# Kernel optimization log

Hardware: AMD Instinct MI355X
Metric: run time of the kernel (lower is better)

The kernel has to match this reference:

```python
import jax, jax.numpy as jnp
import numpy as np

BATCH_SIZE = 2048
TEMPERATURE = 0.5
EPS = 1e-8  # torch CosineSimilarity eps


def setup_inputs() -> dict:
    key = jax.random.key(0)
    k1, k2 = jax.random.split(key)
    d = 512
    z_i = jax.random.normal(k1, (BATCH_SIZE, d), dtype=jnp.float32)
    z_j = jax.random.normal(k2, (BATCH_SIZE, d), dtype=jnp.float32)
    return {"z_i": z_i, "z_j": z_j}


def reference(z_i, z_j):
    B = BATCH_SIZE
    n = 2 * B
    z = jnp.concatenate([z_i, z_j], axis=0)              # [n, d]
    # cosine similarity via normalize + GEMM (same math as broadcasted CosineSimilarity)
    norms = jnp.maximum(jnp.linalg.norm(z, axis=1, keepdims=True), EPS)
    zn = z / norms                                       # [n, d]
    S = zn @ zn.T                                        # [n, n]
    # drop diagonal: row i keeps columns j != i, in order (matches sim[~eye].view(n, n-1))
    cols = jnp.arange(n - 1)[None, :]                    # [1, n-1]
    rows = jnp.arange(n)[:, None]                        # [n, 1]
    idx = cols + (cols >= rows)                          # skip diagonal
    off_diag = jnp.take_along_axis(S, idx, axis=1)       # [n, n-1]
    # positive pair: pos_pairs = cat(z_j, z_i) -> partner index (i + B) mod n
    pos = jnp.take_along_axis(S, ((rows[:, 0] + B) % n)[:, None], axis=1)  # [n, 1]
    logits = jnp.concatenate([pos, off_diag], axis=1) / TEMPERATURE        # [n, n]
    # cross-entropy with label 0, reduction='sum', then / n  == mean over rows
    loss = jnp.mean(jax.nn.logsumexp(logits, axis=1) - logits[:, 0])
    return loss
```

## Files before the change

kernel.cpp:

```cpp
#include <hip/hip_runtime.h>
#include <hip/hip_bf16.h>

#define N_TOT 4096
#define D     512
#define BHALF 2048

#define EXP2_SCALE 2.8853900817779268f
#define E2 7.3890560989306495f

typedef __attribute__((ext_vector_type(8))) short short8;
typedef __attribute__((ext_vector_type(4))) float floatx4;

#define AS_GLOBAL(p) ((const __attribute__((address_space(1))) void*)(p))
#define AS_LDS(p)    ((__attribute__((address_space(3))) void*)(p))

__global__ void normalize_kernel(const float* __restrict__ z_i,
                                 const float* __restrict__ z_j,
                                 short* __restrict__ zn,
                                 float* __restrict__ rowsum) {
    const int wave = threadIdx.x >> 6, lane = threadIdx.x & 63;
    const int row = blockIdx.x * 4 + wave;
    const float* src = (row < BHALF) ? (z_i + (size_t)row * D)
                                     : (z_j + (size_t)(row - BHALF) * D);
    if (lane == 0) rowsum[row] = 0.0f;
    float4 v0 = ((const float4*)src)[lane];
    float4 v1 = ((const float4*)src)[lane + 64];
    float ss = v0.x*v0.x + v0.y*v0.y + v0.z*v0.z + v0.w*v0.w
             + v1.x*v1.x + v1.y*v1.y + v1.z*v1.z + v1.w*v1.w;
    #pragma unroll
    for (int off = 32; off > 0; off >>= 1) ss += __shfl_xor(ss, off);
    float inv = 1.0f / fmaxf(sqrtf(ss), 1e-8f);
    short4 o0, o1;
    o0.x = (short)__bfloat16_as_ushort(__float2bfloat16(v0.x * inv));
    o0.y = (short)__bfloat16_as_ushort(__float2bfloat16(v0.y * inv));
    o0.z = (short)__bfloat16_as_ushort(__float2bfloat16(v0.z * inv));
    o0.w = (short)__bfloat16_as_ushort(__float2bfloat16(v0.w * inv));
    o1.x = (short)__bfloat16_as_ushort(__float2bfloat16(v1.x * inv));
    o1.y = (short)__bfloat16_as_ushort(__float2bfloat16(v1.y * inv));
    o1.z = (short)__bfloat16_as_ushort(__float2bfloat16(v1.z * inv));
    o1.w = (short)__bfloat16_as_ushort(__float2bfloat16(v1.w * inv));
    ((short4*)(zn + (size_t)row * D))[lane]      = o0;
    ((short4*)(zn + (size_t)row * D))[lane + 64] = o1;
}

__launch_bounds__(256)
__global__ void gemm_fused(const short* __restrict__ zn,
                           float* __restrict__ rowsum,
                           float* __restrict__ spos) {
    __shared__ short At[2][128 * 32];
    __shared__ short Bt[2][128 * 32];

    int b = blockIdx.x, bi = 0, rowlen = 32;
    while (b >= rowlen) { b -= rowlen; rowlen--; bi++; }
    const int bj = bi + b;
    const int i0 = bi * 128;
    const int j0 = bj * 128;

    const int t = threadIdx.x;
    const int lane = t & 63, wave = t >> 6;
    const int wm = wave & 1, wn = wave >> 1;
    const int quad = lane >> 4, l16 = lane & 15;

    const int sr = lane >> 2;
    const int sc = (lane & 3) * 8;
    const short* gA0 = zn + (size_t)(i0 + wave * 32 + sr)      * D + sc;
    const short* gA1 = zn + (size_t)(i0 + wave * 32 + 16 + sr) * D + sc;
    const short* gB0 = zn + (size_t)(j0 + wave * 32 + sr)      * D + sc;
    const short* gB1 = zn + (size_t)(j0 + wave * 32 + 16 + sr) * D + sc;
    const int lo0 = (wave * 32)      * 32;
    const int lo1 = (wave * 32 + 16) * 32;

    floatx4 acc[4][4] = {};

    __builtin_amdgcn_global_load_lds(AS_GLOBAL(gA0), AS_LDS(&At[0][lo0]), 16, 0, 0);
    __builtin_amdgcn_global_load_lds(AS_GLOBAL(gA1), AS_LDS(&At[0][lo1]), 16, 0, 0);
    __builtin_amdgcn_global_load_lds(AS_GLOBAL(gB0), AS_LDS(&Bt[0][lo0]), 16, 0, 0);
    __builtin_amdgcn_global_load_lds(AS_GLOBAL(gB1), AS_LDS(&Bt[0][lo1]), 16, 0, 0);

    for (int kt = 0; kt < 16; ++kt) {
        const int cur = kt & 1;
        __syncthreads();
        if (kt < 15) {
            const int nxt = 1 - cur;
            const int ko = (kt + 1) * 32;
            __builtin_amdgcn_global_load_lds(AS_GLOBAL(gA0 + ko), AS_LDS(&At[nxt][lo0]), 16, 0, 0);
            __builtin_amdgcn_global_load_lds(AS_GLOBAL(gA1 + ko), AS_LDS(&At[nxt][lo1]), 16, 0, 0);
            __builtin_amdgcn_global_load_lds(AS_GLOBAL(gB0 + ko), AS_LDS(&Bt[nxt][lo0]), 16, 0, 0);
            __builtin_amdgcn_global_load_lds(AS_GLOBAL(gB1 + ko), AS_LDS(&Bt[nxt][lo1]), 16, 0, 0);
        }
        short8 af[4], bf[4];
        #pragma unroll
        for (int tm = 0; tm < 4; ++tm)
            af[tm] = *(const short8*)(&At[cur][(wm*64 + tm*16 + l16) * 32 + quad*8]);
        #pragma unroll
        for (int tn = 0; tn < 4; ++tn)
            bf[tn] = *(const short8*)(&Bt[cur][(wn*64 + tn*16 + l16) * 32 + quad*8]);
        #pragma unroll
        for (int tm = 0; tm < 4; ++tm)
            #pragma unroll
            for (int tn = 0; tn < 4; ++tn)
                acc[tm][tn] = __builtin_amdgcn_mfma_f32_16x16x32_bf16(
                    af[tm], bf[tn], acc[tm][tn], 0, 0, 0);
    }

    float cs[4] = {0.f, 0.f, 0.f, 0.f};
    #pragma unroll
    for (int tm = 0; tm < 4; ++tm) {
        float rs[4] = {0.f, 0.f, 0.f, 0.f};
        #pragma unroll
        for (int tn = 0; tn < 4; ++tn)
            #pragma unroll
            for (int r = 0; r < 4; ++r) {
                float e = exp2f(acc[tm][tn][r] * EXP2_SCALE);
                rs[r] += e;
                cs[tn] += e;
            }
        #pragma unroll
        for (int r = 0; r < 4; ++r) {
            float v = rs[r];
            v += __shfl_xor(v, 1);
            v += __shfl_xor(v, 2);
            v += __shfl_xor(v, 4);
            v += __shfl_xor(v, 8);
            if (l16 == 0) {
                int gi = i0 + wm*64 + tm*16 + quad*4 + r;
                atomicAdd(&rowsum[gi], v);
            }
        }
    }
    if (bi != bj) {
        #pragma unroll
        for (int tn = 0; tn < 4; ++tn) {
            float v = cs[tn];
            v += __shfl_xor(v, 16);
            v += __shfl_xor(v, 32);
            if (quad == 0) {
                int gj = j0 + wn*64 + tn*16 + l16;
                atomicAdd(&rowsum[gj], v);
            }
        }
    }
    if (bj == bi + 16) {
        #pragma unroll
        for (int tm = 0; tm < 4; ++tm)
            #pragma unroll
            for (int tn = 0; tn < 4; ++tn)
                #pragma unroll
                for (int r = 0; r < 4; ++r) {
                    int li = wm*64 + tm*16 + quad*4 + r;
                    int lj = wn*64 + tn*16 + l16;
                    if (li == lj) {
                        float s = acc[tm][tn][r];
                        spos[i0 + li]         = s;
                        spos[i0 + li + BHALF] = s;
                    }
                }
    }
}

__global__ void finalize_kernel(const float* __restrict__ rowsum,
                                const float* __restrict__ spos,
                                float* __restrict__ out) {
    int t = threadIdx.x;
    float acc = 0.f;
    for (int i = t; i < N_TOT; i += 1024) {
        float sp = spos[i];
        float denom = rowsum[i] - E2 + exp2f(sp * EXP2_SCALE);
        acc += __logf(denom) - 2.0f * sp;
    }
    #pragma unroll
    for (int off = 32; off > 0; off >>= 1) acc += __shfl_xor(acc, off);
    __shared__ float red[16];
    if ((t & 63) == 0) red[t >> 6] = acc;
    __syncthreads();
    if (t == 0) {
        float s = 0.f;
        #pragma unroll
        for (int w = 0; w < 16; ++w) s += red[w];
        out[0] = s / (float)N_TOT;
    }
}

extern "C" void kernel_launch(void* const* d_in, const int* in_sizes, int n_in,
                              void* d_out, int out_size, void* d_ws, size_t ws_size,
                              hipStream_t stream) {
    const float* z_i = (const float*)d_in[0];
    const float* z_j = (const float*)d_in[1];
    float* out = (float*)d_out;

    char* ws = (char*)d_ws;
    short* zn     = (short*)ws;
    float* rowsum = (float*)(ws + (size_t)N_TOT * D * 2);
    float* spos   = rowsum + N_TOT;

    normalize_kernel<<<N_TOT / 4, 256, 0, stream>>>(z_i, z_j, zn, rowsum);
    gemm_fused<<<(32 * 33) / 2, 256, 0, stream>>>(zn, rowsum, spos);
    finalize_kernel<<<1, 1024, 0, stream>>>(rowsum, spos, out);
}
```

Before: 89.94 us.

## Quantize normalized embeddings to FP8 and use triple-buffered FP8 MFMA GEMM

```diff
diff --git a/kernel.cpp b/kernel.cpp
--- a/kernel.cpp
+++ b/kernel.cpp
@@ -8,15 +8,16 @@
 #define EXP2_SCALE 2.8853900817779268f
 #define E2 7.3890560989306495f
 
-typedef __attribute__((ext_vector_type(8))) short short8;
 typedef __attribute__((ext_vector_type(4))) float floatx4;
 
 #define AS_GLOBAL(p) ((const __attribute__((address_space(1))) void*)(p))
 #define AS_LDS(p)    ((__attribute__((address_space(3))) void*)(p))
 
+#define WAITCNT_VM(n) (0xF70 | (n))
+
 __global__ void normalize_kernel(const float* __restrict__ z_i,
                                  const float* __restrict__ z_j,
-                                 short* __restrict__ zn,
+                                 unsigned char* __restrict__ zn,
                                  float* __restrict__ rowsum) {
     const int wave = threadIdx.x >> 6, lane = threadIdx.x & 63;
     const int row = blockIdx.x * 4 + wave;
@@ -30,25 +31,21 @@
     #pragma unroll
     for (int off = 32; off > 0; off >>= 1) ss += __shfl_xor(ss, off);
     float inv = 1.0f / fmaxf(sqrtf(ss), 1e-8f);
-    short4 o0, o1;
-    o0.x = (short)__bfloat16_as_ushort(__float2bfloat16(v0.x * inv));
-    o0.y = (short)__bfloat16_as_ushort(__float2bfloat16(v0.y * inv));
-    o0.z = (short)__bfloat16_as_ushort(__float2bfloat16(v0.z * inv));
-    o0.w = (short)__bfloat16_as_ushort(__float2bfloat16(v0.w * inv));
-    o1.x = (short)__bfloat16_as_ushort(__float2bfloat16(v1.x * inv));
-    o1.y = (short)__bfloat16_as_ushort(__float2bfloat16(v1.y * inv));
-    o1.z = (short)__bfloat16_as_ushort(__float2bfloat16(v1.z * inv));
-    o1.w = (short)__bfloat16_as_ushort(__float2bfloat16(v1.w * inv));
-    ((short4*)(zn + (size_t)row * D))[lane]      = o0;
-    ((short4*)(zn + (size_t)row * D))[lane + 64] = o1;
+    int w0 = __builtin_amdgcn_cvt_pk_fp8_f32(v0.x * inv, v0.y * inv, 0, false);
+    w0     = __builtin_amdgcn_cvt_pk_fp8_f32(v0.z * inv, v0.w * inv, w0, true);
+    int w1 = __builtin_amdgcn_cvt_pk_fp8_f32(v1.x * inv, v1.y * inv, 0, false);
+    w1     = __builtin_amdgcn_cvt_pk_fp8_f32(v1.z * inv, v1.w * inv, w1, true);
+    int* dst = (int*)(zn + (size_t)row * D);
+    dst[lane]      = w0;
+    dst[lane + 64] = w1;
 }
 
 __launch_bounds__(256)
-__global__ void gemm_fused(const short* __restrict__ zn,
+__global__ void gemm_fused(const unsigned char* __restrict__ zn,
                            float* __restrict__ rowsum,
                            float* __restrict__ spos) {
-    __shared__ short At[2][128 * 32];
-    __shared__ short Bt[2][128 * 32];
+    __shared__ unsigned char At[3][128 * 32];
+    __shared__ unsigned char Bt[3][128 * 32];
 
     int b = blockIdx.x, bi = 0, rowlen = 32;
     while (b >= rowlen) { b -= rowlen; rowlen--; bi++; }
@@ -61,45 +58,44 @@
     const int wm = wave & 1, wn = wave >> 1;
     const int quad = lane >> 4, l16 = lane & 15;
 
-    const int sr = lane >> 2;
-    const int sc = (lane & 3) * 8;
-    const short* gA0 = zn + (size_t)(i0 + wave * 32 + sr)      * D + sc;
-    const short* gA1 = zn + (size_t)(i0 + wave * 32 + 16 + sr) * D + sc;
-    const short* gB0 = zn + (size_t)(j0 + wave * 32 + sr)      * D + sc;
-    const short* gB1 = zn + (size_t)(j0 + wave * 32 + 16 + sr) * D + sc;
-    const int lo0 = (wave * 32)      * 32;
-    const int lo1 = (wave * 32 + 16) * 32;
+    const int srow = wave * 32 + (lane >> 1);
+    const int scol = (lane & 1) * 16;
+    const unsigned char* gA = zn + (size_t)(i0 + srow) * D + scol;
+    const unsigned char* gB = zn + (size_t)(j0 + srow) * D + scol;
+    const int lo = srow * 32 + scol;
 
     floatx4 acc[4][4] = {};
 
-    __builtin_amdgcn_global_load_lds(AS_GLOBAL(gA0), AS_LDS(&At[0][lo0]), 16, 0, 0);
-    __builtin_amdgcn_global_load_lds(AS_GLOBAL(gA1), AS_LDS(&At[0][lo1]), 16, 0, 0);
-    __builtin_amdgcn_global_load_lds(AS_GLOBAL(gB0), AS_LDS(&Bt[0][lo0]), 16, 0, 0);
-    __builtin_amdgcn_global_load_lds(AS_GLOBAL(gB1), AS_LDS(&Bt[0][lo1]), 16, 0, 0);
+    __builtin_amdgcn_global_load_lds(AS_GLOBAL(gA),      AS_LDS(&At[0][lo]), 16, 0, 0);
+    __builtin_amdgcn_global_load_lds(AS_GLOBAL(gB),      AS_LDS(&Bt[0][lo]), 16, 0, 0);
+    __builtin_amdgcn_global_load_lds(AS_GLOBAL(gA + 32), AS_LDS(&At[1][lo]), 16, 0, 0);
+    __builtin_amdgcn_global_load_lds(AS_GLOBAL(gB + 32), AS_LDS(&Bt[1][lo]), 16, 0, 0);
 
+    #pragma unroll
     for (int kt = 0; kt < 16; ++kt) {
-        const int cur = kt & 1;
-        __syncthreads();
-        if (kt < 15) {
-            const int nxt = 1 - cur;
-            const int ko = (kt + 1) * 32;
-            __builtin_amdgcn_global_load_lds(AS_GLOBAL(gA0 + ko), AS_LDS(&At[nxt][lo0]), 16, 0, 0);
-            __builtin_amdgcn_global_load_lds(AS_GLOBAL(gA1 + ko), AS_LDS(&At[nxt][lo1]), 16, 0, 0);
-            __builtin_amdgcn_global_load_lds(AS_GLOBAL(gB0 + ko), AS_LDS(&Bt[nxt][lo0]), 16, 0, 0);
-            __builtin_amdgcn_global_load_lds(AS_GLOBAL(gB1 + ko), AS_LDS(&Bt[nxt][lo1]), 16, 0, 0);
+        const int cur = kt % 3;
+        if (kt < 15) __builtin_amdgcn_s_waitcnt(WAITCNT_VM(2));
+        else         __builtin_amdgcn_s_waitcnt(WAITCNT_VM(0));
+        __builtin_amdgcn_s_barrier();
+        __asm__ volatile("" ::: "memory");
+        if (kt < 14) {
+            const int nxt = (kt + 2) % 3;
+            const int ko = (kt + 2) * 32;
+            __builtin_amdgcn_global_load_lds(AS_GLOBAL(gA + ko), AS_LDS(&At[nxt][lo]), 16, 0, 0);
+            __builtin_amdgcn_global_load_lds(AS_GLOBAL(gB + ko), AS_LDS(&Bt[nxt][lo]), 16, 0, 0);
         }
-        short8 af[4], bf[4];
+        long af[4], bf[4];
         #pragma unroll
         for (int tm = 0; tm < 4; ++tm)
-            af[tm] = *(const short8*)(&At[cur][(wm*64 + tm*16 + l16) * 32 + quad*8]);
+            af[tm] = *(const long*)(&At[cur][(wm*64 + tm*16 + l16) * 32 + quad*8]);
         #pragma unroll
         for (int tn = 0; tn < 4; ++tn)
-            bf[tn] = *(const short8*)(&Bt[cur][(wn*64 + tn*16 + l16) * 32 + quad*8]);
+            bf[tn] = *(const long*)(&Bt[cur][(wn*64 + tn*16 + l16) * 32 + quad*8]);
         #pragma unroll
         for (int tm = 0; tm < 4; ++tm)
             #pragma unroll
             for (int tn = 0; tn < 4; ++tn)
-                acc[tm][tn] = __builtin_amdgcn_mfma_f32_16x16x32_bf16(
+                acc[tm][tn] = __builtin_amdgcn_mfma_f32_16x16x32_fp8_fp8(
                     af[tm], bf[tn], acc[tm][tn], 0, 0, 0);
     }
 
@@ -189,8 +185,8 @@
     float* out = (float*)d_out;
 
     char* ws = (char*)d_ws;
-    short* zn     = (short*)ws;
-    float* rowsum = (float*)(ws + (size_t)N_TOT * D * 2);
+    unsigned char* zn = (unsigned char*)ws;
+    float* rowsum = (float*)(ws + (size_t)N_TOT * D);
     float* spos   = rowsum + N_TOT;
 
     normalize_kernel<<<N_TOT / 4, 256, 0, stream>>>(z_i, z_j, zn, rowsum);
```

Measured after the change: 89.80 us. Within noise of the previous version (-0.2%).
